# Kernel optimization log

Measured on AMD Instinct MI355X. Metric: run time of the kernel, lower is better.

## Reference

```python
import jax, jax.numpy as jnp
import numpy as np

B, S, D, H = 4, 512, 768, 200


def setup_inputs() -> dict:
    key = jax.random.key(0)
    ks = jax.random.split(key, 6)
    x = jax.random.normal(ks[0], (B, S, D), dtype=jnp.float32)
    # Linear default init ~ U(-1/sqrt(fan_in), 1/sqrt(fan_in)); scaled normal is fine for a baseline
    W_head = jax.random.normal(ks[1], (D, H), dtype=jnp.float32) * (1.0 / np.sqrt(D))
    b_head = jnp.zeros((H,), dtype=jnp.float32)
    W_tail = jax.random.normal(ks[2], (D, H), dtype=jnp.float32) * (1.0 / np.sqrt(D))
    b_tail = jnp.zeros((H,), dtype=jnp.float32)
    # xavier_normal on [200,200,200]: fan_in = fan_out = 200*200 -> std = sqrt(2/80000)
    U = jax.random.normal(ks[3], (H, H, H), dtype=jnp.float32) * np.sqrt(2.0 / (2 * H * H))
    W_down = jax.random.normal(ks[4], (H, 1), dtype=jnp.float32) * (1.0 / np.sqrt(H))
    b_down = jnp.zeros((1,), dtype=jnp.float32)
    return {"x": x, "W_head": W_head, "b_head": b_head, "W_tail": W_tail,
            "b_tail": b_tail, "U": U, "W_down": W_down, "b_down": b_down}


def reference(x, W_head, b_head, W_tail, b_tail, U, W_down, b_down):
    # head/tail projections with ReLU: [B,S,H]
    head = jax.nn.relu(x @ W_head + b_head)
    tail = jax.nn.relu(x @ W_tail + b_tail)
    # biaffine: 'bxi,oij,byj->bxyo' done as two contractions
    tmp = jnp.einsum('bxi,oij->bxoj', head, U)            # [B,S,H,H]
    logits = jnp.einsum('bxoj,byj->bxyo', tmp, tail)       # [B,S,S,H] (== permuted boxy)
    # down_layer(200->1).squeeze(-1); rope branch in source is dead (rope_logits = 0)
    scores = (logits @ W_down)[..., 0] + b_down[0]         # [B,S,S]
    return scores / jnp.sqrt(jnp.asarray(200.0, dtype=scores.dtype))
```

## Files before the change

kernel.cpp:

```cpp
#include <hip/hip_runtime.h>

#define H 200
#define D 768
#define BATCH 4
#define S 512
#define M (BATCH*S)
#define KP 224
#define NP 208
#define NCAT 400
#define NC4 (H*H/4)
#define VT_BLOCKS 313
#define PREP_BLOCKS 1000

typedef __attribute__((ext_vector_type(8))) short bf16x8;
typedef __attribute__((ext_vector_type(4))) float f32x4;
typedef unsigned short us;

__device__ inline us f2bf(float f) {
    union { float f; unsigned u; } v; v.f = f;
    return (us)((v.u + 0x7FFF + ((v.u >> 16) & 1)) >> 16);
}

__global__ __launch_bounds__(256) void prep(
        const float* __restrict__ x,  const float* __restrict__ Wh,
        const float* __restrict__ Wt, const float* __restrict__ U,
        const float* __restrict__ Wd,
        us* __restrict__ xb, us* __restrict__ Wcb, us* __restrict__ VTb,
        us* __restrict__ headb, us* __restrict__ tailb, us* __restrict__ hvb) {
    int bid = blockIdx.x;
    if (bid < VT_BLOCKS) {
        __shared__ float4 red[8][32];
        int cl = threadIdx.x & 31, q = threadIdx.x >> 5;
        int c = bid * 32 + cl;
        const float4* U4 = (const float4*)U;
        float4 acc = make_float4(0.f, 0.f, 0.f, 0.f);
        if (c < NC4) {
            int o0 = q * 25;
            #pragma unroll
            for (int o = o0; o < o0 + 25; ++o) {
                float w = Wd[o];
                float4 u = U4[(size_t)o * NC4 + c];
                acc.x += w * u.x; acc.y += w * u.y;
                acc.z += w * u.z; acc.w += w * u.w;
            }
        }
        red[q][cl] = acc;
        __syncthreads();
        if (q == 0 && c < NC4) {
            #pragma unroll
            for (int g = 1; g < 8; ++g) {
                float4 r = red[g][cl];
                acc.x += r.x; acc.y += r.y; acc.z += r.z; acc.w += r.w;
            }
            int i = c / (H / 4), j0 = (c % (H / 4)) * 4;
            VTb[(j0 + 0) * KP + i] = f2bf(acc.x);
            VTb[(j0 + 1) * KP + i] = f2bf(acc.y);
            VTb[(j0 + 2) * KP + i] = f2bf(acc.z);
            VTb[(j0 + 3) * KP + i] = f2bf(acc.w);
        }
        return;
    }
    const int GTH = (PREP_BLOCKS - VT_BLOCKS) * 256;
    int gtid = (bid - VT_BLOCKS) * 256 + threadIdx.x;
    {
        const float4* x4 = (const float4*)x;
        ushort4* xb4 = (ushort4*)xb;
        for (int t = gtid; t < M * D / 4; t += GTH) {
            float4 v = x4[t];
            ushort4 o; o.x = f2bf(v.x); o.y = f2bf(v.y); o.z = f2bf(v.z); o.w = f2bf(v.w);
            xb4[t] = o;
        }
    }
    for (int id = gtid; id < NCAT * D; id += GTH) {
        int n = id / D, k = id % D;
        float v = (n < H) ? Wh[k * H + n] : Wt[k * H + (n - H)];
        Wcb[id] = f2bf(v);
    }
    for (int id = gtid; id < M * (KP - H); id += GTH) {
        int r = id / (KP - H), c = H + id % (KP - H);
        headb[r * KP + c] = 0; tailb[r * KP + c] = 0;
    }
    for (int id = gtid; id < M * (KP - NP); id += GTH) {
        int r = id / (KP - NP), c = NP + id % (KP - NP);
        hvb[r * KP + c] = 0;
    }
    for (int id = gtid; id < H * (KP - H); id += GTH) {
        int n = id / (KP - H), k = H + id % (KP - H);
        VTb[n * KP + k] = 0;
    }
    for (int id = gtid; id < (NP - H) * KP; id += GTH) {
        int n = H + id / KP, k = id % KP;
        VTb[n * KP + k] = 0;
    }
}

__global__ __launch_bounds__(64) void proj_mfma(
        const us* __restrict__ xb, const us* __restrict__ Wcb,
        const float* __restrict__ bh, const float* __restrict__ bt,
        us* __restrict__ headb, us* __restrict__ tailb) {
    int lane = threadIdx.x, quad = lane >> 4, col = lane & 15;
    int m0 = blockIdx.x * 32, n0 = blockIdx.y * 16;
    const bf16x8* A0 = (const bf16x8*)(xb + (m0 + col) * D + quad * 8);
    const bf16x8* A1 = (const bf16x8*)(xb + (m0 + 16 + col) * D + quad * 8);
    const bf16x8* Bp = (const bf16x8*)(Wcb + (n0 + col) * D + quad * 8);
    f32x4 acc0 = {0.f,0.f,0.f,0.f}, acc1 = {0.f,0.f,0.f,0.f};
    #pragma unroll 4
    for (int kk = 0; kk < D / 32; ++kk) {
        bf16x8 a0 = A0[kk * 4];
        bf16x8 a1 = A1[kk * 4];
        bf16x8 b  = Bp[kk * 4];
        acc0 = __builtin_amdgcn_mfma_f32_16x16x32_bf16(a0, b, acc0, 0, 0, 0);
        acc1 = __builtin_amdgcn_mfma_f32_16x16x32_bf16(a1, b, acc1, 0, 0, 0);
    }
    int n = n0 + col;
    bool ish = (n < H);
    float bias = ish ? bh[n] : bt[n - H];
    us* dst = ish ? headb : tailb;
    int nn = ish ? n : n - H;
    #pragma unroll
    for (int r = 0; r < 4; ++r) {
        int ma = m0 + quad * 4 + r;
        dst[ma * KP + nn]        = f2bf(fmaxf(acc0[r] + bias, 0.f));
        dst[(ma + 16) * KP + nn] = f2bf(fmaxf(acc1[r] + bias, 0.f));
    }
}

__global__ __launch_bounds__(64) void hv_mfma(
        const us* __restrict__ headb, const us* __restrict__ VTb,
        us* __restrict__ hvb) {
    int lane = threadIdx.x, quad = lane >> 4, col = lane & 15;
    int m0 = blockIdx.x * 32, n0 = blockIdx.y * 16;
    const bf16x8* A0 = (const bf16x8*)(headb + (m0 + col) * KP + quad * 8);
    const bf16x8* A1 = (const bf16x8*)(headb + (m0 + 16 + col) * KP + quad * 8);
    const bf16x8* Bp = (const bf16x8*)(VTb + (n0 + col) * KP + quad * 8);
    f32x4 acc0 = {0.f,0.f,0.f,0.f}, acc1 = {0.f,0.f,0.f,0.f};
    #pragma unroll
    for (int kk = 0; kk < KP / 32; ++kk) {
        bf16x8 a0 = A0[kk * 4];
        bf16x8 a1 = A1[kk * 4];
        bf16x8 b  = Bp[kk * 4];
        acc0 = __builtin_amdgcn_mfma_f32_16x16x32_bf16(a0, b, acc0, 0, 0, 0);
        acc1 = __builtin_amdgcn_mfma_f32_16x16x32_bf16(a1, b, acc1, 0, 0, 0);
    }
    int n = n0 + col;
    #pragma unroll
    for (int r = 0; r < 4; ++r) {
        int ma = m0 + quad * 4 + r;
        hvb[ma * KP + n]        = f2bf(acc0[r]);
        hvb[(ma + 16) * KP + n] = f2bf(acc1[r]);
    }
}

__global__ __launch_bounds__(64) void scores_mfma(
        const us* __restrict__ hvb, const us* __restrict__ tailb,
        const float* __restrict__ bd, float* __restrict__ out) {
    int lane = threadIdx.x, quad = lane >> 4, col = lane & 15;
    int b = blockIdx.z;
    int m0 = blockIdx.x * 32, n0 = blockIdx.y * 32;
    const us* A  = hvb   + (size_t)b * S * KP;
    const us* Bm = tailb + (size_t)b * S * KP;
    const bf16x8* A0 = (const bf16x8*)(A  + (m0 + col) * KP + quad * 8);
    const bf16x8* A1 = (const bf16x8*)(A  + (m0 + 16 + col) * KP + quad * 8);
    const bf16x8* B0 = (const bf16x8*)(Bm + (n0 + col) * KP + quad * 8);
    const bf16x8* B1 = (const bf16x8*)(Bm + (n0 + 16 + col) * KP + quad * 8);
    f32x4 a00 = {0.f,0.f,0.f,0.f}, a01 = {0.f,0.f,0.f,0.f};
    f32x4 a10 = {0.f,0.f,0.f,0.f}, a11 = {0.f,0.f,0.f,0.f};
    #pragma unroll
    for (int kk = 0; kk < KP / 32; ++kk) {
        bf16x8 a0 = A0[kk * 4];
        bf16x8 a1 = A1[kk * 4];
        bf16x8 b0 = B0[kk * 4];
        bf16x8 b1 = B1[kk * 4];
        a00 = __builtin_amdgcn_mfma_f32_16x16x32_bf16(a0, b0, a00, 0, 0, 0);
        a01 = __builtin_amdgcn_mfma_f32_16x16x32_bf16(a0, b1, a01, 0, 0, 0);
        a10 = __builtin_amdgcn_mfma_f32_16x16x32_bf16(a1, b0, a10, 0, 0, 0);
        a11 = __builtin_amdgcn_mfma_f32_16x16x32_bf16(a1, b1, a11, 0, 0, 0);
    }
    float bias = bd[0];
    const float scale = 0.07071067811865475f;
    float* outb = out + (size_t)b * S * S;
    #pragma unroll
    for (int r = 0; r < 4; ++r) {
        int ma = m0 + quad * 4 + r, mb = ma + 16;
        outb[ma * S + n0 + col]      = (a00[r] + bias) * scale;
        outb[ma * S + n0 + 16 + col] = (a01[r] + bias) * scale;
        outb[mb * S + n0 + col]      = (a10[r] + bias) * scale;
        outb[mb * S + n0 + 16 + col] = (a11[r] + bias) * scale;
    }
}

extern "C" void kernel_launch(void* const* d_in, const int* in_sizes, int n_in,
                              void* d_out, int out_size, void* d_ws, size_t ws_size,
                              hipStream_t stream) {
    const float* x  = (const float*)d_in[0];
    const float* Wh = (const float*)d_in[1];
    const float* bh = (const float*)d_in[2];
    const float* Wt = (const float*)d_in[3];
    const float* bt = (const float*)d_in[4];
    const float* U  = (const float*)d_in[5];
    const float* Wd = (const float*)d_in[6];
    const float* bd = (const float*)d_in[7];
    float* out = (float*)d_out;

    us* xb    = (us*)d_ws;
    us* Wcb   = xb    + (size_t)M * D;
    us* VTb   = Wcb   + (size_t)NCAT * D;
    us* hvb   = VTb   + (size_t)NP * KP;
    us* headb = hvb   + (size_t)M * KP;
    us* tailb = headb + (size_t)M * KP;

    prep<<<PREP_BLOCKS, 256, 0, stream>>>(x, Wh, Wt, U, Wd,
                                          xb, Wcb, VTb, headb, tailb, hvb);
    proj_mfma<<<dim3(M / 32, NCAT / 16), 64, 0, stream>>>(xb, Wcb, bh, bt, headb, tailb);
    hv_mfma<<<dim3(M / 32, NP / 16), 64, 0, stream>>>(headb, VTb, hvb);
    scores_mfma<<<dim3(S / 32, S / 32, BATCH), 64, 0, stream>>>(hvb, tailb, bd, out);
}
```

Before: 117.0 us.

## Fuse head-V projection into scores kernel via LDS staging

Merges the hv GEMM and the scores GEMM into one kernel. Each block computes its 32 rows of head·V into shared memory and then reuses them for 8 column tiles of scores. This removes the global hvb buffer round-trip, its padding initialization, and one kernel launch. In exchange, the hv work is computed redundantly across the two y-blocks, and the grid shrinks to 128 larger blocks, which reduces wave-level parallelism.

```diff
diff --git a/kernel.cpp b/kernel.cpp
--- a/kernel.cpp
+++ b/kernel.cpp
@@ -6,11 +6,11 @@
 #define S 512
 #define M (BATCH*S)
 #define KP 224
-#define NP 208
 #define NCAT 400
 #define NC4 (H*H/4)
 #define VT_BLOCKS 313
 #define PREP_BLOCKS 1000
+#define LDSK 232
 
 typedef __attribute__((ext_vector_type(8))) short bf16x8;
 typedef __attribute__((ext_vector_type(4))) float f32x4;
@@ -26,7 +26,7 @@
         const float* __restrict__ Wt, const float* __restrict__ U,
         const float* __restrict__ Wd,
         us* __restrict__ xb, us* __restrict__ Wcb, us* __restrict__ VTb,
-        us* __restrict__ headb, us* __restrict__ tailb, us* __restrict__ hvb) {
+        us* __restrict__ headb, us* __restrict__ tailb) {
     int bid = blockIdx.x;
     if (bid < VT_BLOCKS) {
         __shared__ float4 red[8][32];
@@ -80,15 +80,11 @@
         int r = id / (KP - H), c = H + id % (KP - H);
         headb[r * KP + c] = 0; tailb[r * KP + c] = 0;
     }
-    for (int id = gtid; id < M * (KP - NP); id += GTH) {
-        int r = id / (KP - NP), c = NP + id % (KP - NP);
-        hvb[r * KP + c] = 0;
-    }
     for (int id = gtid; id < H * (KP - H); id += GTH) {
         int n = id / (KP - H), k = H + id % (KP - H);
         VTb[n * KP + k] = 0;
     }
-    for (int id = gtid; id < (NP - H) * KP; id += GTH) {
+    for (int id = gtid; id < (KP - H) * KP; id += GTH) {
         int n = H + id / KP, k = id % KP;
         VTb[n * KP + k] = 0;
     }
@@ -125,67 +121,71 @@
     }
 }
 
-__global__ __launch_bounds__(64) void hv_mfma(
+__global__ __launch_bounds__(256) void hvscores(
         const us* __restrict__ headb, const us* __restrict__ VTb,
-        us* __restrict__ hvb) {
-    int lane = threadIdx.x, quad = lane >> 4, col = lane & 15;
-    int m0 = blockIdx.x * 32, n0 = blockIdx.y * 16;
-    const bf16x8* A0 = (const bf16x8*)(headb + (m0 + col) * KP + quad * 8);
-    const bf16x8* A1 = (const bf16x8*)(headb + (m0 + 16 + col) * KP + quad * 8);
-    const bf16x8* Bp = (const bf16x8*)(VTb + (n0 + col) * KP + quad * 8);
-    f32x4 acc0 = {0.f,0.f,0.f,0.f}, acc1 = {0.f,0.f,0.f,0.f};
-    #pragma unroll
-    for (int kk = 0; kk < KP / 32; ++kk) {
-        bf16x8 a0 = A0[kk * 4];
-        bf16x8 a1 = A1[kk * 4];
-        bf16x8 b  = Bp[kk * 4];
-        acc0 = __builtin_amdgcn_mfma_f32_16x16x32_bf16(a0, b, acc0, 0, 0, 0);
-        acc1 = __builtin_amdgcn_mfma_f32_16x16x32_bf16(a1, b, acc1, 0, 0, 0);
-    }
-    int n = n0 + col;
-    #pragma unroll
-    for (int r = 0; r < 4; ++r) {
-        int ma = m0 + quad * 4 + r;
-        hvb[ma * KP + n]        = f2bf(acc0[r]);
-        hvb[(ma + 16) * KP + n] = f2bf(acc1[r]);
-    }
-}
-
-__global__ __launch_bounds__(64) void scores_mfma(
-        const us* __restrict__ hvb, const us* __restrict__ tailb,
-        const float* __restrict__ bd, float* __restrict__ out) {
-    int lane = threadIdx.x, quad = lane >> 4, col = lane & 15;
+        const us* __restrict__ tailb, const float* __restrict__ bd,
+        float* __restrict__ out) {
+    __shared__ us hvs[32 * LDSK];
+    int w = threadIdx.x >> 6, lane = threadIdx.x & 63;
+    int quad = lane >> 4, col = lane & 15;
     int b = blockIdx.z;
-    int m0 = blockIdx.x * 32, n0 = blockIdx.y * 32;
-    const us* A  = hvb   + (size_t)b * S * KP;
-    const us* Bm = tailb + (size_t)b * S * KP;
-    const bf16x8* A0 = (const bf16x8*)(A  + (m0 + col) * KP + quad * 8);
-    const bf16x8* A1 = (const bf16x8*)(A  + (m0 + 16 + col) * KP + quad * 8);
-    const bf16x8* B0 = (const bf16x8*)(Bm + (n0 + col) * KP + quad * 8);
-    const bf16x8* B1 = (const bf16x8*)(Bm + (n0 + 16 + col) * KP + quad * 8);
-    f32x4 a00 = {0.f,0.f,0.f,0.f}, a01 = {0.f,0.f,0.f,0.f};
-    f32x4 a10 = {0.f,0.f,0.f,0.f}, a11 = {0.f,0.f,0.f,0.f};
-    #pragma unroll
-    for (int kk = 0; kk < KP / 32; ++kk) {
-        bf16x8 a0 = A0[kk * 4];
-        bf16x8 a1 = A1[kk * 4];
-        bf16x8 b0 = B0[kk * 4];
-        bf16x8 b1 = B1[kk * 4];
-        a00 = __builtin_amdgcn_mfma_f32_16x16x32_bf16(a0, b0, a00, 0, 0, 0);
-        a01 = __builtin_amdgcn_mfma_f32_16x16x32_bf16(a0, b1, a01, 0, 0, 0);
-        a10 = __builtin_amdgcn_mfma_f32_16x16x32_bf16(a1, b0, a10, 0, 0, 0);
-        a11 = __builtin_amdgcn_mfma_f32_16x16x32_bf16(a1, b1, a11, 0, 0, 0);
-    }
+    int m0 = blockIdx.x * 32;
+    const us* Ah = headb + (size_t)(b * S + m0) * KP;
+
+    const bf16x8* A0 = (const bf16x8*)(Ah + col * KP + quad * 8);
+    const bf16x8* A1 = (const bf16x8*)(Ah + (16 + col) * KP + quad * 8);
+    for (int nt = w; nt < KP / 16; nt += 4) {
+        const bf16x8* Bp = (const bf16x8*)(VTb + (nt * 16 + col) * KP + quad * 8);
+        f32x4 acc0 = {0.f,0.f,0.f,0.f}, acc1 = {0.f,0.f,0.f,0.f};
+        #pragma unroll
+        for (int kk = 0; kk < KP / 32; ++kk) {
+            bf16x8 a0 = A0[kk * 4];
+            bf16x8 a1 = A1[kk * 4];
+            bf16x8 bf = Bp[kk * 4];
+            acc0 = __builtin_amdgcn_mfma_f32_16x16x32_bf16(a0, bf, acc0, 0, 0, 0);
+            acc1 = __builtin_amdgcn_mfma_f32_16x16x32_bf16(a1, bf, acc1, 0, 0, 0);
+        }
+        int n = nt * 16 + col;
+        #pragma unroll
+        for (int r = 0; r < 4; ++r) {
+            hvs[(quad * 4 + r) * LDSK + n]        = f2bf(acc0[r]);
+            hvs[(16 + quad * 4 + r) * LDSK + n]   = f2bf(acc1[r]);
+        }
+    }
+    __syncthreads();
+
+    const us* Bt = tailb + (size_t)b * S * KP;
+    const bf16x8* LA0 = (const bf16x8*)(hvs + col * LDSK + quad * 8);
+    const bf16x8* LA1 = (const bf16x8*)(hvs + (16 + col) * LDSK + quad * 8);
     float bias = bd[0];
     const float scale = 0.07071067811865475f;
     float* outb = out + (size_t)b * S * S;
-    #pragma unroll
-    for (int r = 0; r < 4; ++r) {
-        int ma = m0 + quad * 4 + r, mb = ma + 16;
-        outb[ma * S + n0 + col]      = (a00[r] + bias) * scale;
-        outb[ma * S + n0 + 16 + col] = (a01[r] + bias) * scale;
-        outb[mb * S + n0 + col]      = (a10[r] + bias) * scale;
-        outb[mb * S + n0 + 16 + col] = (a11[r] + bias) * scale;
+    for (int yi = 0; yi < 2; ++yi) {
+        int yt = blockIdx.y * 8 + w + yi * 4;
+        int n0 = yt * 32;
+        const bf16x8* B0 = (const bf16x8*)(Bt + (n0 + col) * KP + quad * 8);
+        const bf16x8* B1 = (const bf16x8*)(Bt + (n0 + 16 + col) * KP + quad * 8);
+        f32x4 a00 = {0.f,0.f,0.f,0.f}, a01 = {0.f,0.f,0.f,0.f};
+        f32x4 a10 = {0.f,0.f,0.f,0.f}, a11 = {0.f,0.f,0.f,0.f};
+        #pragma unroll
+        for (int kk = 0; kk < KP / 32; ++kk) {
+            bf16x8 a0 = LA0[kk * 4];
+            bf16x8 a1 = LA1[kk * 4];
+            bf16x8 b0 = B0[kk * 4];
+            bf16x8 b1 = B1[kk * 4];
+            a00 = __builtin_amdgcn_mfma_f32_16x16x32_bf16(a0, b0, a00, 0, 0, 0);
+            a01 = __builtin_amdgcn_mfma_f32_16x16x32_bf16(a0, b1, a01, 0, 0, 0);
+            a10 = __builtin_amdgcn_mfma_f32_16x16x32_bf16(a1, b0, a10, 0, 0, 0);
+            a11 = __builtin_amdgcn_mfma_f32_16x16x32_bf16(a1, b1, a11, 0, 0, 0);
+        }
+        #pragma unroll
+        for (int r = 0; r < 4; ++r) {
+            int ma = m0 + quad * 4 + r, mb = ma + 16;
+            outb[ma * S + n0 + col]      = (a00[r] + bias) * scale;
+            outb[ma * S + n0 + 16 + col] = (a01[r] + bias) * scale;
+            outb[mb * S + n0 + col]      = (a10[r] + bias) * scale;
+            outb[mb * S + n0 + 16 + col] = (a11[r] + bias) * scale;
+        }
     }
 }
 
@@ -205,13 +205,11 @@
     us* xb    = (us*)d_ws;
     us* Wcb   = xb    + (size_t)M * D;
     us* VTb   = Wcb   + (size_t)NCAT * D;
-    us* hvb   = VTb   + (size_t)NP * KP;
-    us* headb = hvb   + (size_t)M * KP;
+    us* headb = VTb   + (size_t)KP * KP;
     us* tailb = headb + (size_t)M * KP;
 
     prep<<<PREP_BLOCKS, 256, 0, stream>>>(x, Wh, Wt, U, Wd,
-                                          xb, Wcb, VTb, headb, tailb, hvb);
+                                          xb, Wcb, VTb, headb, tailb);
     proj_mfma<<<dim3(M / 32, NCAT / 16), 64, 0, stream>>>(xb, Wcb, bh, bt, headb, tailb);
-    hv_mfma<<<dim3(M / 32, NP / 16), 64, 0, stream>>>(headb, VTb, hvb);
-    scores_mfma<<<dim3(S / 32, S / 32, BATCH), 64, 0, stream>>>(hvb, tailb, bd, out);
-}
+    hvscores<<<dim3(S / 32, 2, BATCH), 256, 0, stream>>>(headb, VTb, tailb, bd, out);
+}
```

New measurement: 125.2 us. +7.0%, slower.
